# Performance work log

Hardware: AMD Instinct MI355X
Metric: run time of the kernel (lower is better)

## Reference

```python
import jax, jax.numpy as jnp
import numpy as np

WINDOW_SIZE = 11
C1 = 0.01 ** 2
C2 = 0.03 ** 2


def _box_filter(x, ws):
    # x: [B,1,H,W]; uniform box filter, zero padding (== torch conv2d pad=ws//2)
    k = jnp.full((1, 1, ws, ws), 1.0 / (ws * ws), dtype=x.dtype)
    pad = ws // 2
    return jax.lax.conv_general_dilated(
        x, k, window_strides=(1, 1), padding=[(pad, pad), (pad, pad)],
        dimension_numbers=('NCHW', 'OIHW', 'NCHW'))


def setup_inputs() -> dict:
    key = jax.random.key(0)
    k1, k2 = jax.random.split(key)
    img1 = jax.random.uniform(k1, (64, 1, 512, 512), dtype=jnp.float32)
    img2 = jax.random.uniform(k2, (64, 1, 512, 512), dtype=jnp.float32)
    return {"img1": img1, "img2": img2}


def reference(img1, img2):
    ws = WINDOW_SIZE
    mu1 = _box_filter(img1, ws)
    mu2 = _box_filter(img2, ws)
    mu1_sq = mu1 * mu1
    mu2_sq = mu2 * mu2
    mu1_mu2 = mu1 * mu2
    sigma1_sq = _box_filter(img1 * img1, ws) - mu1_sq
    sigma2_sq = _box_filter(img2 * img2, ws) - mu2_sq
    sigma12 = _box_filter(img1 * img2, ws) - mu1_mu2
    ssim_map = ((2 * mu1_mu2 + C1) * (2 * sigma12 + C2)) / (
        (mu1_sq + mu2_sq + C1) * (sigma1_sq + sigma2_sq + C2))
    return 1.0 - jnp.mean(ssim_map)
```

## Files before the change

### kernel.cpp

```cpp
#include <hip/hip_runtime.h>


#define IMG_H 512
#define IMG_W 512
#define N_IMG 64
#define STRIP 32
#define NTHREADS 256
#define LDSW (IMG_W + 10)

__global__ __launch_bounds__(NTHREADS) void ssim_kernel(const float* __restrict__ img1,
                                                        const float* __restrict__ img2,
                                                        float* __restrict__ ws) {
    __shared__ float V[2][5][LDSW];
    const int t = threadIdx.x;
    const int b = blockIdx.y;
    const int r0 = blockIdx.x * STRIP;
    const float* __restrict__ p1 = img1 + (size_t)b * (IMG_H * IMG_W);
    const float* __restrict__ p2 = img2 + (size_t)b * (IMG_H * IMG_W);

    for (int i = t; i < 2 * 5 * LDSW; i += NTHREADS) (&V[0][0][0])[i] = 0.0f;

    const int c0 = t;
    const int c1 = t + NTHREADS;

    float cs[5][2];
#pragma unroll
    for (int ch = 0; ch < 5; ++ch) { cs[ch][0] = 0.f; cs[ch][1] = 0.f; }

    auto add_row = [&](int r) {
        const float* row1 = p1 + r * IMG_W;
        const float* row2 = p2 + r * IMG_W;
        float x0 = row1[c0], y0 = row2[c0];
        float x1 = row1[c1], y1 = row2[c1];
        cs[0][0] += x0;                       cs[0][1] += x1;
        cs[1][0] += y0;                       cs[1][1] += y1;
        cs[2][0] = fmaf(x0, x0, cs[2][0]);    cs[2][1] = fmaf(x1, x1, cs[2][1]);
        cs[3][0] = fmaf(y0, y0, cs[3][0]);    cs[3][1] = fmaf(y1, y1, cs[3][1]);
        cs[4][0] = fmaf(x0, y0, cs[4][0]);    cs[4][1] = fmaf(x1, y1, cs[4][1]);
    };
    auto sub_row = [&](int r) {
        const float* row1 = p1 + r * IMG_W;
        const float* row2 = p2 + r * IMG_W;
        float x0 = row1[c0], y0 = row2[c0];
        float x1 = row1[c1], y1 = row2[c1];
        cs[0][0] -= x0;                       cs[0][1] -= x1;
        cs[1][0] -= y0;                       cs[1][1] -= y1;
        cs[2][0] = fmaf(-x0, x0, cs[2][0]);   cs[2][1] = fmaf(-x1, x1, cs[2][1]);
        cs[3][0] = fmaf(-y0, y0, cs[3][0]);   cs[3][1] = fmaf(-y1, y1, cs[3][1]);
        cs[4][0] = fmaf(-x0, y0, cs[4][0]);   cs[4][1] = fmaf(-x1, y1, cs[4][1]);
    };

    {
        int rlo = r0 - 5; if (rlo < 0) rlo = 0;
        int rhi = r0 + 5; if (rhi > IMG_H - 1) rhi = IMG_H - 1;
        for (int r = rlo; r <= rhi; ++r) add_row(r);
    }

    __syncthreads();

    constexpr float inv = 1.0f / 121.0f;
    constexpr float C1v = 0.01f * 0.01f;
    constexpr float C2v = 0.03f * 0.03f;
    float acc = 0.0f;

    for (int rr = 0; rr < STRIP; ++rr) {
        const int r = r0 + rr;
        if (rr > 0) {
            int ri = r + 5;
            int ro = r - 6;
            if (ri < IMG_H) add_row(ri);
            if (ro >= 0)    sub_row(ro);
        }

        float (*buf)[LDSW] = V[rr & 1];
#pragma unroll
        for (int ch = 0; ch < 5; ++ch) {
            buf[ch][5 + c0] = cs[ch][0];
            buf[ch][5 + c1] = cs[ch][1];
        }
        __syncthreads();

#pragma unroll
        for (int k = 0; k < 2; ++k) {
            const int c = (k == 0) ? c0 : c1;
            float h[5];
#pragma unroll
            for (int ch = 0; ch < 5; ++ch) {
                float s = 0.f;
#pragma unroll
                for (int j = 0; j < 11; ++j) s += buf[ch][c + j];
                h[ch] = s;
            }
            float mu1 = h[0] * inv, mu2 = h[1] * inv;
            float mu1mu2 = mu1 * mu2, mu1sq = mu1 * mu1, mu2sq = mu2 * mu2;
            float s12 = fmaf(h[4], inv, -mu1mu2);
            float s11 = fmaf(h[2], inv, -mu1sq);
            float s22 = fmaf(h[3], inv, -mu2sq);
            float num = (2.f * mu1mu2 + C1v) * (2.f * s12 + C2v);
            float den = (mu1sq + mu2sq + C1v) * (s11 + s22 + C2v);
            acc += __fdividef(num, den);
        }
    }

#pragma unroll
    for (int off = 32; off > 0; off >>= 1) acc += __shfl_down(acc, off);
    __shared__ float wsum[4];
    if ((t & 63) == 0) wsum[t >> 6] = acc;
    __syncthreads();
    if (t == 0) atomicAdd(ws, wsum[0] + wsum[1] + wsum[2] + wsum[3]);
}

__global__ void ssim_finalize(const float* __restrict__ ws, float* __restrict__ out) {
    constexpr float inv_n = 1.0f / (float)((size_t)N_IMG * IMG_H * IMG_W);
    out[0] = 1.0f - ws[0] * inv_n;
}

extern "C" void kernel_launch(void* const* d_in, const int* in_sizes, int n_in,
                              void* d_out, int out_size, void* d_ws, size_t ws_size,
                              hipStream_t stream) {
    const float* img1 = (const float*)d_in[0];
    const float* img2 = (const float*)d_in[1];
    float* out = (float*)d_out;
    float* ws = (float*)d_ws;

    hipMemsetAsync(ws, 0, sizeof(float), stream);

    dim3 grid(IMG_H / STRIP, N_IMG);
    ssim_kernel<<<grid, NTHREADS, 0, stream>>>(img1, img2, ws);
    ssim_finalize<<<1, 1, 0, stream>>>(ws, out);
}
```

Before: 203.8 us.

## Batch vertical sums into 4-row LDS chunks and slide horizontal window per thread

Each thread now loads two adjacent columns with float2, and vertical column sums for 4 rows are staged in LDS before one barrier. Each wave then computes one row's horizontal box sums: a thread covers 8 consecutive columns with float4 LDS reads and a running sliding-window sum instead of 11 adds per output. Strips grow to 64 rows, which halves halo recomputation but also halves the grid to 512 blocks. LDS use grows to about 42KB per block, which may reduce occupancy.

```diff
diff --git a/kernel.cpp b/kernel.cpp
--- a/kernel.cpp
+++ b/kernel.cpp
@@ -4,107 +4,102 @@
 #define IMG_H 512
 #define IMG_W 512
 #define N_IMG 64
-#define STRIP 32
+#define STRIP 64
+#define CHUNK 4
 #define NTHREADS 256
-#define LDSW (IMG_W + 10)
+#define LDSW 524
 
 __global__ __launch_bounds__(NTHREADS) void ssim_kernel(const float* __restrict__ img1,
                                                         const float* __restrict__ img2,
                                                         float* __restrict__ ws) {
-    __shared__ float V[2][5][LDSW];
+    __shared__ float V[CHUNK][5][LDSW];
+    __shared__ float wsum[4];
     const int t = threadIdx.x;
     const int b = blockIdx.y;
     const int r0 = blockIdx.x * STRIP;
     const float* __restrict__ p1 = img1 + (size_t)b * (IMG_H * IMG_W);
     const float* __restrict__ p2 = img2 + (size_t)b * (IMG_H * IMG_W);
 
-    for (int i = t; i < 2 * 5 * LDSW; i += NTHREADS) (&V[0][0][0])[i] = 0.0f;
+    for (int i = t; i < CHUNK * 5 * LDSW; i += NTHREADS) (&V[0][0][0])[i] = 0.0f;
 
-    const int c0 = t;
-    const int c1 = t + NTHREADS;
-
+    const int c = 2 * t;
     float cs[5][2];
 #pragma unroll
     for (int ch = 0; ch < 5; ++ch) { cs[ch][0] = 0.f; cs[ch][1] = 0.f; }
 
-    auto add_row = [&](int r) {
-        const float* row1 = p1 + r * IMG_W;
-        const float* row2 = p2 + r * IMG_W;
-        float x0 = row1[c0], y0 = row2[c0];
-        float x1 = row1[c1], y1 = row2[c1];
-        cs[0][0] += x0;                       cs[0][1] += x1;
-        cs[1][0] += y0;                       cs[1][1] += y1;
-        cs[2][0] = fmaf(x0, x0, cs[2][0]);    cs[2][1] = fmaf(x1, x1, cs[2][1]);
-        cs[3][0] = fmaf(y0, y0, cs[3][0]);    cs[3][1] = fmaf(y1, y1, cs[3][1]);
-        cs[4][0] = fmaf(x0, y0, cs[4][0]);    cs[4][1] = fmaf(x1, y1, cs[4][1]);
-    };
-    auto sub_row = [&](int r) {
-        const float* row1 = p1 + r * IMG_W;
-        const float* row2 = p2 + r * IMG_W;
-        float x0 = row1[c0], y0 = row2[c0];
-        float x1 = row1[c1], y1 = row2[c1];
-        cs[0][0] -= x0;                       cs[0][1] -= x1;
-        cs[1][0] -= y0;                       cs[1][1] -= y1;
-        cs[2][0] = fmaf(-x0, x0, cs[2][0]);   cs[2][1] = fmaf(-x1, x1, cs[2][1]);
-        cs[3][0] = fmaf(-y0, y0, cs[3][0]);   cs[3][1] = fmaf(-y1, y1, cs[3][1]);
-        cs[4][0] = fmaf(-x0, y0, cs[4][0]);   cs[4][1] = fmaf(-x1, y1, cs[4][1]);
+    auto roll = [&](int r, float sign) {
+        float2 x = *(const float2*)(p1 + (size_t)r * IMG_W + c);
+        float2 y = *(const float2*)(p2 + (size_t)r * IMG_W + c);
+        float sx0 = sign * x.x, sx1 = sign * x.y;
+        float sy0 = sign * y.x, sy1 = sign * y.y;
+        cs[0][0] += sx0;                     cs[0][1] += sx1;
+        cs[1][0] += sy0;                     cs[1][1] += sy1;
+        cs[2][0] = fmaf(sx0, x.x, cs[2][0]); cs[2][1] = fmaf(sx1, x.y, cs[2][1]);
+        cs[3][0] = fmaf(sy0, y.x, cs[3][0]); cs[3][1] = fmaf(sy1, y.y, cs[3][1]);
+        cs[4][0] = fmaf(sx0, y.x, cs[4][0]); cs[4][1] = fmaf(sx1, y.y, cs[4][1]);
     };
 
     {
         int rlo = r0 - 5; if (rlo < 0) rlo = 0;
         int rhi = r0 + 5; if (rhi > IMG_H - 1) rhi = IMG_H - 1;
-        for (int r = rlo; r <= rhi; ++r) add_row(r);
+        for (int r = rlo; r <= rhi; ++r) roll(r, 1.0f);
     }
 
     __syncthreads();
 
+    const int seg = t & 63;
+    const int hrow = t >> 6;
     constexpr float inv = 1.0f / 121.0f;
     constexpr float C1v = 0.01f * 0.01f;
     constexpr float C2v = 0.03f * 0.03f;
     float acc = 0.0f;
 
-    for (int rr = 0; rr < STRIP; ++rr) {
-        const int r = r0 + rr;
-        if (rr > 0) {
-            int ri = r + 5;
-            int ro = r - 6;
-            if (ri < IMG_H) add_row(ri);
-            if (ro >= 0)    sub_row(ro);
-        }
-
-        float (*buf)[LDSW] = V[rr & 1];
+    for (int rc = r0; rc < r0 + STRIP; rc += CHUNK) {
+        for (int q = 0; q < CHUNK; ++q) {
+            int r = rc + q;
+            if (r > r0) {
+                int ri = r + 5, ro = r - 6;
+                if (ri < IMG_H) roll(ri, 1.0f);
+                if (ro >= 0)    roll(ro, -1.0f);
+            }
 #pragma unroll
-        for (int ch = 0; ch < 5; ++ch) {
-            buf[ch][5 + c0] = cs[ch][0];
-            buf[ch][5 + c1] = cs[ch][1];
+            for (int ch = 0; ch < 5; ++ch)
+                *(float2*)&V[q][ch][6 + c] = make_float2(cs[ch][0], cs[ch][1]);
         }
         __syncthreads();
 
-#pragma unroll
-        for (int k = 0; k < 2; ++k) {
-            const int c = (k == 0) ? c0 : c1;
-            float h[5];
+        {
+            float h[5][8];
 #pragma unroll
             for (int ch = 0; ch < 5; ++ch) {
-                float s = 0.f;
+                float buf[20];
+                const float4* src = (const float4*)&V[hrow][ch][8 * seg];
 #pragma unroll
-                for (int j = 0; j < 11; ++j) s += buf[ch][c + j];
-                h[ch] = s;
+                for (int i = 0; i < 5; ++i) ((float4*)buf)[i] = src[i];
+                float w = 0.f;
+#pragma unroll
+                for (int j = 1; j <= 11; ++j) w += buf[j];
+                h[ch][0] = w;
+#pragma unroll
+                for (int k = 1; k < 8; ++k) { w += buf[k + 11] - buf[k]; h[ch][k] = w; }
             }
-            float mu1 = h[0] * inv, mu2 = h[1] * inv;
-            float mu1mu2 = mu1 * mu2, mu1sq = mu1 * mu1, mu2sq = mu2 * mu2;
-            float s12 = fmaf(h[4], inv, -mu1mu2);
-            float s11 = fmaf(h[2], inv, -mu1sq);
-            float s22 = fmaf(h[3], inv, -mu2sq);
-            float num = (2.f * mu1mu2 + C1v) * (2.f * s12 + C2v);
-            float den = (mu1sq + mu2sq + C1v) * (s11 + s22 + C2v);
-            acc += __fdividef(num, den);
+#pragma unroll
+            for (int k = 0; k < 8; ++k) {
+                float mu1 = h[0][k] * inv, mu2 = h[1][k] * inv;
+                float m12 = mu1 * mu2, m11 = mu1 * mu1, m22 = mu2 * mu2;
+                float s12 = fmaf(h[4][k], inv, -m12);
+                float s11 = fmaf(h[2][k], inv, -m11);
+                float s22 = fmaf(h[3][k], inv, -m22);
+                float num = (2.f * m12 + C1v) * (2.f * s12 + C2v);
+                float den = (m11 + m22 + C1v) * (s11 + s22 + C2v);
+                acc += __fdividef(num, den);
+            }
         }
+        __syncthreads();
     }
 
 #pragma unroll
     for (int off = 32; off > 0; off >>= 1) acc += __shfl_down(acc, off);
-    __shared__ float wsum[4];
     if ((t & 63) == 0) wsum[t >> 6] = acc;
     __syncthreads();
     if (t == 0) atomicAdd(ws, wsum[0] + wsum[1] + wsum[2] + wsum[3]);
```

New measurement: 267.3 us. 1.31x slower.
